# Optimization experiments

Hardware: AMD Instinct MI355X
Metric: run time of the kernel (lower is better)

The kernel has to match this reference:

```python
import jax, jax.numpy as jnp
import numpy as np
from jax import lax
from math import sqrt

STYLE_DIM = 512
K = 3


def _equal_linear(latent, w, b):
    # EqualLinear: runtime weight scaling by 1/sqrt(fan_in)
    scale = 1.0 / sqrt(latent.shape[1])
    return latent @ (w.T * scale) + b


def _pixel_norm(x, axis=1, eps=1e-8):
    return x * jax.lax.rsqrt(jnp.mean(x * x, axis=axis, keepdims=True) + eps)


def _modconv(x, latent, weight, bias, el_w, el_b):
    # weight: (nc2, nc1, 3, 3); x: (B, nc1, H, W); latent: (B, style_dim)
    b = x.shape[0]
    nc2, nc1, k, _ = weight.shape
    fan_in = nc1 * k * k
    w = weight * sqrt(2.0 / fan_in)                      # (nc2, nc1, 3, 3)
    # style: s = 1 + PixelNorm(EqualLinear(latent))      # (B, nc1)
    s = 1.0 + _pixel_norm(_equal_linear(latent, el_w, el_b), axis=1)
    # demod: d_bo = rsqrt(sum_{c,k} (s_bc * w_ock)^2 + 1e-5)
    wsq = jnp.sum(w * w, axis=(2, 3))                    # (nc2, nc1)
    d = jax.lax.rsqrt(jnp.einsum('bc,oc->bo', s * s, wsq) + 1e-5)  # (B, nc2)
    # conv(x, s*w)*d  ==  conv(s*x, w)*d  (s is per input channel)
    xm = x * s[:, :, None, None]
    y = lax.conv_general_dilated(
        xm, w, window_strides=(1, 1), padding=[(1, 1), (1, 1)],
        dimension_numbers=('NCHW', 'OIHW', 'NCHW'))
    return y * d[:, :, None, None] + bias


def _style_block(x, latent, w0, b0, el0_w, el0_b, w1, b1, el1_w, el1_b):
    act_gain = sqrt(2.0)
    out = _modconv(x, latent, w0, b0, el0_w, el0_b)
    out = jax.nn.leaky_relu(out, 0.2) * act_gain
    out = _pixel_norm(out, axis=1)
    out = _modconv(out, latent, w1, b1, el1_w, el1_b)
    out = jax.nn.leaky_relu(out, 0.2) * act_gain
    out = _pixel_norm(out, axis=1)
    return out


def setup_inputs() -> dict:
    key = jax.random.key(0)
    ks = jax.random.split(key, 8)
    B, NC1, NC2, H, W = 8, 256, 256, 128, 128
    return {
        'x': jax.random.normal(ks[0], (B, NC1, H, W), jnp.float32),
        'latent': jax.random.normal(ks[1], (B, STYLE_DIM), jnp.float32),
        'w0': jax.random.normal(ks[2], (NC2, NC1, K, K), jnp.float32),
        'b0': jnp.zeros((1, NC2, 1, 1), jnp.float32),
        'el0_w': jax.random.normal(ks[3], (NC1, STYLE_DIM), jnp.float32),
        'el0_b': jnp.zeros((NC1,), jnp.float32),
        'w1': jax.random.normal(ks[4], (NC2, NC2, K, K), jnp.float32),
        'b1': jnp.zeros((1, NC2, 1, 1), jnp.float32),
        'el1_w': jax.random.normal(ks[5], (NC2, STYLE_DIM), jnp.float32),
        'el1_b': jnp.zeros((NC2,), jnp.float32),
    }


def reference(x, latent, w0, b0, el0_w, el0_b, w1, b1, el1_w, el1_b):
    return _style_block(x, latent, w0, b0, el0_w, el0_b, w1, b1, el1_w, el1_b)
```

## Files before the change

### kernel.cpp

```cpp
#include <hip/hip_runtime.h>
#include <hip/hip_bf16.h>

typedef __attribute__((ext_vector_type(8))) short short8;
typedef __attribute__((ext_vector_type(16))) float f32x16;

typedef const __attribute__((address_space(1))) unsigned int* gas1_t;
typedef __attribute__((address_space(3))) unsigned int* las3_t;

__device__ __forceinline__ unsigned short f2bf(float x) {
    unsigned int u = __float_as_uint(x);
    u = (u + 0x7fffu + ((u >> 16) & 1u)) >> 16;
    return (unsigned short)u;
}

__device__ __forceinline__ int4 pack8(const unsigned short* u) {
    int4 p;
    p.x = (int)((unsigned)u[0] | ((unsigned)u[1] << 16));
    p.y = (int)((unsigned)u[2] | ((unsigned)u[3] << 16));
    p.z = (int)((unsigned)u[4] | ((unsigned)u[5] << 16));
    p.w = (int)((unsigned)u[6] | ((unsigned)u[7] << 16));
    return p;
}

__device__ __forceinline__ void gld_lds16(const void* g, void* l) {
    __builtin_amdgcn_global_load_lds((gas1_t)g, (las3_t)l, 16, 0, 0);
}

__global__ void style_kernel(const float* __restrict__ latent,
                             const float* __restrict__ elw0, const float* __restrict__ elb0,
                             const float* __restrict__ elw1, const float* __restrict__ elb1,
                             float* __restrict__ s_arr) {
    const int cv = blockIdx.x >> 3;
    const int b  = blockIdx.x & 7;
    const int c  = threadIdx.x;
    const float* elw = cv ? elw1 : elw0;
    const float* elb = cv ? elb1 : elb0;

    __shared__ float lat[512];
    lat[c] = latent[b * 512 + c];
    lat[c + 256] = latent[b * 512 + c + 256];
    __syncthreads();

    float accv = 0.f;
    const float* wrow = elw + (size_t)c * 512;
#pragma unroll 8
    for (int k = 0; k < 512; ++k) accv += lat[k] * wrow[k];
    const float lin = accv * 0.04419417382415922f + elb[c];

    float sq = lin * lin;
#pragma unroll
    for (int off = 32; off >= 1; off >>= 1) sq += __shfl_xor(sq, off);
    __shared__ float wsum[4];
    if ((threadIdx.x & 63) == 0) wsum[threadIdx.x >> 6] = sq;
    __syncthreads();
    const float total = wsum[0] + wsum[1] + wsum[2] + wsum[3];
    const float s = 1.0f + lin * rsqrtf(total * (1.0f / 256.0f) + 1e-8f);
    s_arr[(cv * 8 + b) * 256 + c] = s;
}

__global__ void wsq_kernel(const float* __restrict__ w0, const float* __restrict__ w1,
                           float* __restrict__ wsq) {
    const int cv = blockIdx.x >> 8;
    const int o  = blockIdx.x & 255;
    const int c  = threadIdx.x;
    const float* w = cv ? w1 : w0;
    const size_t base = ((size_t)o * 256 + c) * 9;
    float ssum = 0.f;
#pragma unroll
    for (int t = 0; t < 9; ++t) { float v = w[base + t]; ssum += v * v; }
    wsq[((size_t)cv * 256 + o) * 256 + c] = ssum * (2.0f / 2304.0f);
}

__global__ void demod_kernel(const float* __restrict__ s_arr, const float* __restrict__ wsq,
                             float* __restrict__ d_arr) {
    const int cv = blockIdx.x >> 3;
    const int b  = blockIdx.x & 7;
    const int o  = threadIdx.x;
    __shared__ float ss[256];
    float sv = s_arr[(cv * 8 + b) * 256 + o];
    ss[o] = sv * sv;
    __syncthreads();
    const float* wrow = wsq + ((size_t)cv * 256 + o) * 256;
    float accv = 0.f;
#pragma unroll 8
    for (int c = 0; c < 256; ++c) accv += ss[c] * wrow[c];
    d_arr[(cv * 8 + b) * 256 + o] = rsqrtf(accv + 1e-5f);
}

__global__ void fold_kernel(const float* __restrict__ w0, const float* __restrict__ w1,
                            const float* __restrict__ s_arr, const float* __restrict__ d_arr,
                            unsigned short* __restrict__ wm0, unsigned short* __restrict__ wm1) {
    const int cv = blockIdx.y;
    const int e  = blockIdx.x * 256 + threadIdx.x;
    const float* w = cv ? w1 : w0;
    unsigned short* wm = cv ? wm1 : wm0;
    const int slab = e >> 13;
    const int idx  = e & 8191;
    const int b  = slab / 72;
    const int s2 = slab - b * 72;
    const int cc = s2 / 9;
    const int t  = s2 - cc * 9;
    const int o  = idx >> 5;
    const int c5 = idx & 31;
    const int c  = cc * 32 + c5;
    const float val = w[((size_t)o * 256 + c) * 9 + t] * 0.029462782549439483f
                    * s_arr[(cv * 8 + b) * 256 + c] * d_arr[(cv * 8 + b) * 256 + o];
    wm[((size_t)slab << 13) + (c5 >> 3) * 2048 + o * 8 + (c5 & 7)] = f2bf(val);
}

__global__ void convert_kernel(const float* __restrict__ x, unsigned short* __restrict__ xq) {
    const int blk = blockIdx.x;
    const int hh  = blk & 127;
    const int bg_ = blk >> 7;
    const int g   = bg_ & 31;
    const int b   = bg_ >> 5;
    __shared__ float sx[8][128];
    const int tid = threadIdx.x;
#pragma unroll
    for (int i = 0; i < 4; ++i) {
        const int idx = tid + i * 256;
        const int c8 = idx >> 7, p = idx & 127;
        sx[c8][p] = x[(((size_t)b * 256 + g * 8 + c8) * 128 + hh) * 128 + p];
    }
    __syncthreads();
    if (tid < 128) {
        const int p = tid;
        unsigned short u[8];
#pragma unroll
        for (int j = 0; j < 8; ++j) u[j] = f2bf(sx[j][p]);
        *(int4*)(xq + ((((size_t)b * 32 + g) * 128 + hh) * 128 + p) * 8) = pack8(u);
    }
}

template<bool FINAL_OUT>
__global__ __launch_bounds__(1024, 4) void conv_kernel(
    const unsigned short* __restrict__ in_q, const unsigned short* __restrict__ wmod,
    const float* __restrict__ bias, const unsigned short* __restrict__ zpg,
    void* __restrict__ out_v) {

    __shared__ __align__(16) char lds[136256];

    const int tid  = threadIdx.x;
    const int b    = blockIdx.x & 7;
    const int rp   = blockIdx.x >> 3;
    const int h0   = rp * 2;
    const int lane = tid & 63;
    const int wr   = tid >> 6;
    const int wm   = wr & 3;
    const int wn2  = (wr >> 2) & 1;
    const int wrow = wr >> 3;
    const int l31  = lane & 31;
    const int khg  = lane >> 5;

    float* sbias = (float*)(lds + 131136);
    if (tid < 256) sbias[tid] = bias[tid];
    if (tid < 4)   *(int4*)(lds + 131072 + tid * 16) = (int4){0, 0, 0, 0};

    int aoff[2][2];
#pragma unroll
    for (int mb = 0; mb < 2; ++mb)
#pragma unroll
        for (int kh = 0; kh < 2; ++kh)
            aoff[mb][kh] = ((khg + 2 * kh) * 256 + wm * 64 + mb * 32 + l31) * 16;
    int boff[2][2];
#pragma unroll
    for (int nb = 0; nb < 2; ++nb)
#pragma unroll
        for (int kh = 0; kh < 2; ++kh)
            boff[nb][kh] = 98304 + (khg + 2 * kh) * 2048
                         + (wn2 * 64 + nb * 32 + l31) * 16;
    const bool isL = (wn2 == 0) && (l31 == 0);
    const bool isR = (wn2 == 1) && (l31 == 31);

    const unsigned short* wmb = wmod + (size_t)b * 589824;
    const unsigned short* xqb = in_q + (size_t)b * 4194304;

    auto issueA3 = [&](const char* src, int nbuf) {
        char* db = lds + nbuf * 49152 + wr * 1024;
        const char* s = src + wr * 1024 + lane * 16;
#pragma unroll
        for (int j = 0; j < 3; ++j)
            gld_lds16(s + j * 16384, db + j * 16384);
    };

    auto issueBrows = [&](int cc, int r0, int r1) {
        const int row = wr >> 2;
        if (row < r0 || row >= r1) return;
        const int koct = wr & 3;
        char* dst = lds + 98304 + row * 8192 + koct * 2048;
        const int hin = h0 - 1 + row;
        if ((unsigned)hin < 128u) {
            const unsigned short* src = xqb
                + ((size_t)(cc * 4 + koct) * 128 + hin) * 1024 + lane * 8;
            gld_lds16(src,       dst);
            gld_lds16(src + 512, dst + 1024);
        } else {
            gld_lds16(zpg, dst);
            gld_lds16(zpg, dst + 1024);
        }
    };

    f32x16 acc[2][2];
#pragma unroll
    for (int mb = 0; mb < 2; ++mb)
#pragma unroll
        for (int nb = 0; nb < 2; ++nb)
#pragma unroll
            for (int r = 0; r < 16; ++r) acc[mb][nb][r] = 0.f;

    issueA3((const char*)wmb, 0);
    issueBrows(0, 0, 4);
    __syncthreads();

    const char* gA = (const char*)wmb + 49152;
#pragma unroll 1
    for (int cc = 0; cc < 8; ++cc) {
#pragma unroll
        for (int r = 0; r < 3; ++r) {
            const int g = cc * 3 + r;
            if (r == 0 && cc > 0) issueBrows(cc, 2, 4);
            if (r == 2 && cc < 7) issueBrows(cc + 1, 0, 2);
            if (g < 23) { issueA3(gA, (g + 1) & 1); gA += 49152; }
            const char* Ac = lds + (g & 1) * 49152;
#pragma unroll
            for (int i = 0; i < 3; ++i) {
                short8 af[2][2], bf[2][2];
#pragma unroll
                for (int mb = 0; mb < 2; ++mb)
#pragma unroll
                    for (int kh = 0; kh < 2; ++kh)
                        af[mb][kh] = *(const short8*)(Ac + i * 16384 + aoff[mb][kh]);
                const int badd = (wrow + r) * 8192 + (i - 1) * 16;
#pragma unroll
                for (int nb = 0; nb < 2; ++nb)
#pragma unroll
                    for (int kh = 0; kh < 2; ++kh) {
                        int off = boff[nb][kh] + badd;
                        if (i == 0 && nb == 0) off = isL ? 131072 : off;
                        if (i == 2 && nb == 1) off = isR ? 131072 : off;
                        bf[nb][kh] = *(const short8*)(lds + off);
                    }
#pragma unroll
                for (int kh = 0; kh < 2; ++kh)
#pragma unroll
                    for (int mb = 0; mb < 2; ++mb)
#pragma unroll
                        for (int nb = 0; nb < 2; ++nb)
                            acc[mb][nb] = __builtin_amdgcn_mfma_f32_32x32x16_bf16(
                                af[mb][kh], bf[nb][kh], acc[mb][nb], 0, 0, 0);
            }
            asm volatile("s_waitcnt vmcnt(0) lgkmcnt(0)" ::: "memory");
            __builtin_amdgcn_sched_barrier(0);
            __builtin_amdgcn_s_barrier();
        }
    }

    float psum[2] = {0.f, 0.f};
    const float actGain = 1.4142135623730951f;
#pragma unroll
    for (int mb = 0; mb < 2; ++mb)
#pragma unroll
        for (int rg = 0; rg < 16; ++rg) {
            const int row = (rg & 3) + 8 * (rg >> 2) + 4 * khg;
            const float bo = sbias[wm * 64 + mb * 32 + row];
#pragma unroll
            for (int nb = 0; nb < 2; ++nb) {
                float v = acc[mb][nb][rg] + bo;
                v = (v > 0.f ? v : 0.2f * v) * actGain;
                acc[mb][nb][rg] = v;
                psum[nb] += v * v;
            }
        }
    psum[0] += __shfl_xor(psum[0], 32);
    psum[1] += __shfl_xor(psum[1], 32);
    float* red = (float*)(lds + 132160);
    const int rslot = (wrow * 2 + wn2) * 4 + wm;
    if (lane < 32) {
        red[rslot * 64 + l31]      = psum[0];
        red[rslot * 64 + 32 + l31] = psum[1];
    }
    __syncthreads();
    float rs[2];
#pragma unroll
    for (int nb = 0; nb < 2; ++nb) {
        const int p = nb * 32 + l31;
        const int base = (wrow * 2 + wn2) * 4;
        const float ssum = red[(base + 0) * 64 + p] + red[(base + 1) * 64 + p]
                         + red[(base + 2) * 64 + p] + red[(base + 3) * 64 + p];
        rs[nb] = rsqrtf(ssum * (1.0f / 256.0f) + 1e-8f);
    }

    const int h = h0 + wrow;
    if (FINAL_OUT) {
        float* outF = (float*)out_v;
#pragma unroll
        for (int mb = 0; mb < 2; ++mb)
#pragma unroll
            for (int rg = 0; rg < 16; ++rg) {
                const int row = (rg & 3) + 8 * (rg >> 2) + 4 * khg;
                const int o = wm * 64 + mb * 32 + row;
                const size_t rb = (((size_t)b * 256 + o) * 128 + h) * 128 + wn2 * 64;
#pragma unroll
                for (int nb = 0; nb < 2; ++nb)
                    outF[rb + nb * 32 + l31] = acc[mb][nb][rg] * rs[nb];
            }
    } else {
        unsigned short* outB = (unsigned short*)out_v;
        char* wreg = lds + wr * 4096;
#pragma unroll
        for (int mb = 0; mb < 2; ++mb) {
#pragma unroll
            for (int rg = 0; rg < 16; rg += 2) {
                const int row = (rg & 3) + 8 * (rg >> 2) + 4 * khg;
#pragma unroll
                for (int nb = 0; nb < 2; ++nb) {
                    const int pxl = nb * 32 + l31;
                    const unsigned lo = f2bf(acc[mb][nb][rg]     * rs[nb]);
                    const unsigned hi = f2bf(acc[mb][nb][rg + 1] * rs[nb]);
                    *(unsigned int*)(wreg + pxl * 64 + (((row >> 3) ^ (pxl & 3)) << 4)
                                     + (row & 7) * 2) = lo | (hi << 16);
                }
            }
            asm volatile("s_waitcnt lgkmcnt(0)" ::: "memory");
#pragma unroll
            for (int oc = 0; oc < 4; ++oc) {
                const int pxl = lane;
                const int4 v = *(const int4*)(wreg + pxl * 64 + ((oc ^ (pxl & 3)) << 4));
                const int gch = wm * 8 + mb * 4 + oc;
                *(int4*)(outB + ((((size_t)b * 32 + gch) * 128 + h) * 128
                                 + wn2 * 64 + pxl) * 8) = v;
            }
            asm volatile("s_waitcnt lgkmcnt(0)" ::: "memory");
        }
    }
}

extern "C" void kernel_launch(void* const* d_in, const int* in_sizes, int n_in,
                              void* d_out, int out_size, void* d_ws, size_t ws_size,
                              hipStream_t stream) {
    (void)in_sizes; (void)n_in; (void)out_size; (void)ws_size;
    const float* x      = (const float*)d_in[0];
    const float* latent = (const float*)d_in[1];
    const float* w0     = (const float*)d_in[2];
    const float* b0     = (const float*)d_in[3];
    const float* el0w   = (const float*)d_in[4];
    const float* el0b   = (const float*)d_in[5];
    const float* w1     = (const float*)d_in[6];
    const float* b1     = (const float*)d_in[7];
    const float* el1w   = (const float*)d_in[8];
    const float* el1b   = (const float*)d_in[9];

    char* ws = (char*)d_ws;
    float* s_arr = (float*)ws;
    float* d_arr = (float*)(ws + 16384);
    float* wsq   = (float*)(ws + 32768);
    unsigned short* zpg = (unsigned short*)(ws + 32768);
    unsigned short* wm0 = (unsigned short*)(ws + 557056);
    unsigned short* wm1 = (unsigned short*)(ws + 9994240);
    unsigned short* xq  = (unsigned short*)(ws + 19431424);
    unsigned short* tmp = (unsigned short*)(ws + 86540288);

    style_kernel<<<16, 256, 0, stream>>>(latent, el0w, el0b, el1w, el1b, s_arr);
    wsq_kernel<<<512, 256, 0, stream>>>(w0, w1, wsq);
    demod_kernel<<<16, 256, 0, stream>>>(s_arr, wsq, d_arr);
    hipMemsetAsync(zpg, 0, 256, stream);
    fold_kernel<<<dim3(18432, 2), 256, 0, stream>>>(w0, w1, s_arr, d_arr, wm0, wm1);
    convert_kernel<<<32768, 256, 0, stream>>>(x, xq);

    conv_kernel<false><<<512, 1024, 0, stream>>>(xq, wm0, b0, zpg, tmp);
    conv_kernel<true><<<512, 1024, 0, stream>>>(tmp, wm1, b1, zpg, d_out);
}
```

Measured before the change: 370.7 us.

## Load modulated weights directly from global into registers instead of LDS

```diff
diff --git a/kernel.cpp b/kernel.cpp
--- a/kernel.cpp
+++ b/kernel.cpp
@@ -138,7 +138,7 @@
     const float* __restrict__ bias, const unsigned short* __restrict__ zpg,
     void* __restrict__ out_v) {
 
-    __shared__ __align__(16) char lds[136256];
+    __shared__ __align__(16) char lds[65536];
 
     const int tid  = threadIdx.x;
     const int b    = blockIdx.x & 7;
@@ -152,42 +152,37 @@
     const int l31  = lane & 31;
     const int khg  = lane >> 5;
 
-    float* sbias = (float*)(lds + 131136);
+    float* sbias = (float*)(lds + 32832);
     if (tid < 256) sbias[tid] = bias[tid];
-    if (tid < 4)   *(int4*)(lds + 131072 + tid * 16) = (int4){0, 0, 0, 0};
-
-    int aoff[2][2];
-#pragma unroll
-    for (int mb = 0; mb < 2; ++mb)
+    if (tid < 4)   *(int4*)(lds + 32768 + tid * 16) = (int4){0, 0, 0, 0};
+
+    int boff[2][2];
+#pragma unroll
+    for (int nb = 0; nb < 2; ++nb)
 #pragma unroll
         for (int kh = 0; kh < 2; ++kh)
-            aoff[mb][kh] = ((khg + 2 * kh) * 256 + wm * 64 + mb * 32 + l31) * 16;
-    int boff[2][2];
-#pragma unroll
-    for (int nb = 0; nb < 2; ++nb)
-#pragma unroll
-        for (int kh = 0; kh < 2; ++kh)
-            boff[nb][kh] = 98304 + (khg + 2 * kh) * 2048
+            boff[nb][kh] = (khg + 2 * kh) * 2048
                          + (wn2 * 64 + nb * 32 + l31) * 16;
     const bool isL = (wn2 == 0) && (l31 == 0);
     const bool isR = (wn2 == 1) && (l31 == 31);
 
     const unsigned short* wmb = wmod + (size_t)b * 589824;
     const unsigned short* xqb = in_q + (size_t)b * 4194304;
-
-    auto issueA3 = [&](const char* src, int nbuf) {
-        char* db = lds + nbuf * 49152 + wr * 1024;
-        const char* s = src + wr * 1024 + lane * 16;
-#pragma unroll
-        for (int j = 0; j < 3; ++j)
-            gld_lds16(s + j * 16384, db + j * 16384);
+    const char* aLane = (const char*)wmb + khg * 4096 + (wm * 64 + l31) * 16;
+
+    auto loadA = [&](int slab, short8 (&af)[2][2]) {
+        const char* p = aLane + (size_t)slab * 16384;
+        af[0][0] = *(const short8*)(p);
+        af[1][0] = *(const short8*)(p + 512);
+        af[0][1] = *(const short8*)(p + 8192);
+        af[1][1] = *(const short8*)(p + 8704);
     };
 
     auto issueBrows = [&](int cc, int r0, int r1) {
         const int row = wr >> 2;
         if (row < r0 || row >= r1) return;
         const int koct = wr & 3;
-        char* dst = lds + 98304 + row * 8192 + koct * 2048;
+        char* dst = lds + row * 8192 + koct * 2048;
         const int hin = h0 - 1 + row;
         if ((unsigned)hin < 128u) {
             const unsigned short* src = xqb
@@ -208,11 +203,9 @@
 #pragma unroll
             for (int r = 0; r < 16; ++r) acc[mb][nb][r] = 0.f;
 
-    issueA3((const char*)wmb, 0);
     issueBrows(0, 0, 4);
     __syncthreads();
 
-    const char* gA = (const char*)wmb + 49152;
 #pragma unroll 1
     for (int cc = 0; cc < 8; ++cc) {
 #pragma unroll
@@ -220,24 +213,18 @@
             const int g = cc * 3 + r;
             if (r == 0 && cc > 0) issueBrows(cc, 2, 4);
             if (r == 2 && cc < 7) issueBrows(cc + 1, 0, 2);
-            if (g < 23) { issueA3(gA, (g + 1) & 1); gA += 49152; }
-            const char* Ac = lds + (g & 1) * 49152;
 #pragma unroll
             for (int i = 0; i < 3; ++i) {
                 short8 af[2][2], bf[2][2];
-#pragma unroll
-                for (int mb = 0; mb < 2; ++mb)
-#pragma unroll
-                    for (int kh = 0; kh < 2; ++kh)
-                        af[mb][kh] = *(const short8*)(Ac + i * 16384 + aoff[mb][kh]);
+                loadA(g * 3 + i, af);
                 const int badd = (wrow + r) * 8192 + (i - 1) * 16;
 #pragma unroll
                 for (int nb = 0; nb < 2; ++nb)
 #pragma unroll
                     for (int kh = 0; kh < 2; ++kh) {
                         int off = boff[nb][kh] + badd;
-                        if (i == 0 && nb == 0) off = isL ? 131072 : off;
-                        if (i == 2 && nb == 1) off = isR ? 131072 : off;
+                        if (i == 0 && nb == 0) off = isL ? 32768 : off;
+                        if (i == 2 && nb == 1) off = isR ? 32768 : off;
                         bf[nb][kh] = *(const short8*)(lds + off);
                     }
 #pragma unroll
@@ -273,7 +260,7 @@
         }
     psum[0] += __shfl_xor(psum[0], 32);
     psum[1] += __shfl_xor(psum[1], 32);
-    float* red = (float*)(lds + 132160);
+    float* red = (float*)(lds + 33856);
     const int rslot = (wrow * 2 + wn2) * 4 + wm;
     if (lane < 32) {
         red[rslot * 64 + l31]      = psum[0];
@@ -305,6 +292,7 @@
                     outF[rb + nb * 32 + l31] = acc[mb][nb][rg] * rs[nb];
             }
     } else {
+        __syncthreads();
         unsigned short* outB = (unsigned short*)out_v;
         char* wreg = lds + wr * 4096;
 #pragma unroll
```

Result: slower. 394.4 us (+6.4%).
